# Performance work log

Measured on AMD Instinct MI355X. Metric: run time of the kernel, lower is better.

Reference implementation:

```python
import jax, jax.numpy as jnp
import numpy as np

N_QUMODES = 128
N_LAYERS = 8
BATCH = 131072
HBAR = 2.0  # PennyLane default.gaussian convention; vacuum covariance = I


def setup_inputs() -> dict:
    key = jax.random.key(0)
    k1, k2 = jax.random.split(key)
    inputs = jax.random.normal(k1, (BATCH, N_QUMODES), dtype=jnp.float32)
    params = jax.random.normal(k2, (N_LAYERS, 3 * N_QUMODES), dtype=jnp.float32)
    return {"inputs": inputs, "params": params}


def _rot(theta):
    # Rotation gate on (x, p): x -> c x - s p, p -> s x + c p. Shape [..., 2, 2].
    c, s = jnp.cos(theta), jnp.sin(theta)
    return jnp.stack([jnp.stack([c, -s], -1), jnp.stack([s, c], -1)], -2)


def _build_symplectic(params):
    """Compose the full 2N x 2N symplectic matrix for all layers.

    Per layer: local per-mode blocks R(th2) @ Sq(r) @ R(th1), then a fixed
    chain of pi/4 beamsplitters on modes (0,1),(1,2),...  Quadrature ordering
    is interleaved: (x0, p0, x1, p1, ...).
    """
    N, L = N_QUMODES, N_LAYERS
    p = params.reshape(L, N, 3)
    th1, r, th2 = p[..., 0], p[..., 1], p[..., 2]
    z = jnp.zeros_like(r)
    sq = jnp.stack([jnp.stack([jnp.exp(-r), z], -1),
                    jnp.stack([z, jnp.exp(r)], -1)], -2)  # [L, N, 2, 2]
    blk = jnp.einsum('lnab,lnbc,lncd->lnad', _rot(th2), sq, _rot(th1))

    # Fixed beamsplitter chain matrix C (theta = pi/4, phi = 0).
    t = float(np.cos(np.pi / 4))
    rr = float(np.sin(np.pi / 4))
    BS4 = jnp.array([[t, 0., -rr, 0.],
                     [0., t, 0., -rr],
                     [rr, 0., t, 0.],
                     [0., rr, 0., t]], dtype=params.dtype)
    C = jnp.eye(2 * N, dtype=params.dtype)
    for i in range(N - 1):
        C = C.at[2 * i:2 * i + 4, :].set(BS4 @ C[2 * i:2 * i + 4, :])

    idx = jnp.arange(N)
    S = jnp.eye(2 * N, dtype=params.dtype)
    for l in range(L):
        D = jnp.zeros((N, 2, N, 2), params.dtype).at[idx, :, idx, :].set(blk[l])
        S = C @ (D.reshape(2 * N, 2 * N) @ S)
    return S


def reference(inputs, params):
    """Batched Gaussian simulation of the CV QNN; returns <n_i> per sample."""
    S = _build_symplectic(params)
    B, N = inputs.shape[0], N_QUMODES
    # Displacement(a, 0): mu_x += sqrt(2*hbar) * a = 2a for hbar = 2.
    mu0 = jnp.zeros((B, 2 * N), inputs.dtype).at[:, 0::2].set(2.0 * inputs)
    mu = mu0 @ S.T                      # [B, 2N]
    V = S @ S.T                         # vacuum cov = I -> V = S S^T
    dV = jnp.diagonal(V)
    dsum = dV[0::2] + dV[1::2]          # V_xx + V_pp per mode, [N]
    n = (dsum[None, :] + mu[:, 0::2] ** 2 + mu[:, 1::2] ** 2) / (2.0 * HBAR) - 0.5
    return n
```

## Files before the change

kernel.cpp:

```cpp
#include <hip/hip_runtime.h>


#define BATCH 131072

typedef __attribute__((ext_vector_type(8))) short bf16x8;
typedef __attribute__((ext_vector_type(4))) float f32x4;

#define MFMA(a, b, c) __builtin_amdgcn_mfma_f32_16x16x32_bf16(a, b, c, 0, 0, 0)

__device__ __forceinline__ unsigned short f2bf(float f) {
  unsigned int u = __float_as_uint(f);
  u += 0x7FFFu + ((u >> 16) & 1u);
  return (unsigned short)(u >> 16);
}
__device__ __forceinline__ float bf2f(unsigned short h) {
  return __uint_as_float(((unsigned int)h) << 16);
}
__device__ __forceinline__ void pack8(const float* v, uint4& hv, uint4& lv) {
  unsigned int hw[4], lw[4];
#pragma unroll
  for (int p = 0; p < 4; ++p) {
    unsigned short h0 = f2bf(v[2 * p]), h1 = f2bf(v[2 * p + 1]);
    unsigned short l0 = f2bf(v[2 * p] - bf2f(h0)), l1 = f2bf(v[2 * p + 1] - bf2f(h1));
    hw[p] = (unsigned int)h0 | ((unsigned int)h1 << 16);
    lw[p] = (unsigned int)l0 | ((unsigned int)l1 << 16);
  }
  hv = make_uint4(hw[0], hw[1], hw[2], hw[3]);
  lv = make_uint4(lw[0], lw[1], lw[2], lw[3]);
}

__global__ __launch_bounds__(256) void build_m(const float* __restrict__ params,
                                               unsigned short* __restrict__ Mhi,
                                               unsigned short* __restrict__ Mlo) {
  int bx = blockIdx.x;
  int l = bx >> 8;
  int idx = bx & 255;
  int t = threadIdx.x;
  int i, j;
  if (l & 1) { i = idx; j = t; } else { j = idx; i = t; }
  int a = i >> 1, nn = j >> 1;
  float cx;
  if (a < 127) {
    if (nn == 0) cx = exp2f(-0.5f * (float)(a + 1));
    else if (nn <= a) cx = exp2f(-0.5f * (float)(a - nn + 2));
    else if (nn == a + 1) cx = -0.70710678118654752f;
    else cx = 0.0f;
  } else {
    cx = (nn == 0) ? exp2f(-63.5f) : exp2f(-0.5f * (float)(128 - nn));
  }
  const float* p = params + l * 384 + nn * 3;
  float th1 = p[0], r = p[1], th2 = p[2];
  float c1 = cosf(th1), s1 = sinf(th1);
  float c2 = cosf(th2), s2 = sinf(th2);
  float em = expf(-r), ep = expf(r);
  float bb;
  if (i & 1) bb = (j & 1) ? (-s2 * s1 * em + c2 * c1 * ep) : (s2 * c1 * em + c2 * s1 * ep);
  else       bb = (j & 1) ? (-c2 * s1 * em - s2 * c1 * ep) : (c2 * c1 * em - s2 * s1 * ep);
  float v = cx * bb;
  unsigned short hi = f2bf(v);
  unsigned short lo = f2bf(v - bf2f(hi));
  int off = l * 65536 + ((l & 1) ? (i * 256 + j) : (j * 256 + i));
  Mhi[off] = hi;
  Mlo[off] = lo;
}

#define PSTR 40
__global__ __launch_bounds__(256) void matprod(
    const unsigned short* __restrict__ Lhi_base, const unsigned short* __restrict__ Llo_base,
    const unsigned short* __restrict__ Rhi_base, const unsigned short* __restrict__ Rlo_base,
    unsigned short* __restrict__ Ohi, unsigned short* __restrict__ Olo,
    float* __restrict__ Sout, int final_mode) {
  __shared__ __align__(16) char lds_raw[4 * 128 * PSTR * 2];
  unsigned short* sLhi = (unsigned short*)lds_raw;
  unsigned short* sLlo = sLhi + 128 * PSTR;
  unsigned short* sRhi = sLlo + 128 * PSTR;
  unsigned short* sRlo = sRhi + 128 * PSTR;
  float* sEp = (float*)lds_raw;

  int bx = blockIdx.x;
  int pair = bx >> 2, tile = bx & 3;
  int tr = tile >> 1, tc = tile & 1;
  const unsigned short* Lhi = Lhi_base + (2 * pair + 1) * 65536;
  const unsigned short* Llo = Llo_base + (2 * pair + 1) * 65536;
  const unsigned short* Rhi = Rhi_base + (2 * pair) * 65536;
  const unsigned short* Rlo = Rlo_base + (2 * pair) * 65536;

  int t = threadIdx.x;
  int lane = t & 63, w = t >> 6;
  int wr = (w >> 1) * 64, wc = (w & 1) * 64;
  int l15 = lane & 15, q = lane >> 4;

  f32x4 acc[4][4];
#pragma unroll
  for (int a = 0; a < 4; ++a)
#pragma unroll
    for (int b = 0; b < 4; ++b) acc[a][b] = (f32x4){0.f, 0.f, 0.f, 0.f};

  for (int kc = 0; kc < 256; kc += 32) {
    __syncthreads();
#pragma unroll
    for (int it = 0; it < 2; ++it) {
      int e = it * 2048 + t * 8;
      int row = e >> 5, k = e & 31;
      *(uint4*)(sLhi + row * PSTR + k) = *(const uint4*)(Lhi + (tr * 128 + row) * 256 + kc + k);
      *(uint4*)(sLlo + row * PSTR + k) = *(const uint4*)(Llo + (tr * 128 + row) * 256 + kc + k);
      *(uint4*)(sRhi + row * PSTR + k) = *(const uint4*)(Rhi + (tc * 128 + row) * 256 + kc + k);
      *(uint4*)(sRlo + row * PSTR + k) = *(const uint4*)(Rlo + (tc * 128 + row) * 256 + kc + k);
    }
    __syncthreads();
    int kb = q * 8;
    bf16x8 afh[4], afl[4], bfh[4], bfl[4];
#pragma unroll
    for (int rt = 0; rt < 4; ++rt) {
      int r = wr + rt * 16 + l15;
      afh[rt] = *(const bf16x8*)(sLhi + r * PSTR + kb);
      afl[rt] = *(const bf16x8*)(sLlo + r * PSTR + kb);
      int n = wc + rt * 16 + l15;
      bfh[rt] = *(const bf16x8*)(sRhi + n * PSTR + kb);
      bfl[rt] = *(const bf16x8*)(sRlo + n * PSTR + kb);
    }
#pragma unroll
    for (int rt = 0; rt < 4; ++rt)
#pragma unroll
      for (int ct = 0; ct < 4; ++ct) {
        acc[rt][ct] = MFMA(afh[rt], bfh[ct], acc[rt][ct]);
        acc[rt][ct] = MFMA(afh[rt], bfl[ct], acc[rt][ct]);
        acc[rt][ct] = MFMA(afl[rt], bfh[ct], acc[rt][ct]);
      }
  }

  for (int ph = 0; ph < 2; ++ph) {
    __syncthreads();
    if (wr == ph * 64) {
#pragma unroll
      for (int rt = 0; rt < 4; ++rt)
#pragma unroll
        for (int ct = 0; ct < 4; ++ct) {
          int rl = rt * 16 + q * 4;
          int col = wc + ct * 16 + l15;
#pragma unroll
          for (int rg = 0; rg < 4; ++rg) sEp[(rl + rg) * 129 + col] = acc[rt][ct][rg];
        }
    }
    __syncthreads();
    if (final_mode) {
      int rl = t >> 2, cseg = (t & 3) * 32;
      for (int cc = 0; cc < 32; cc += 4) {
        int c = cseg + cc;
        *(float4*)(Sout + (tr * 128 + ph * 64 + rl) * 256 + tc * 128 + c) =
            make_float4(sEp[rl * 129 + c], sEp[rl * 129 + c + 1],
                        sEp[rl * 129 + c + 2], sEp[rl * 129 + c + 3]);
      }
    } else if (pair & 1) {
      int rl = t >> 2, cseg = (t & 3) * 32;
      for (int cc = 0; cc < 32; cc += 8) {
        float v[8];
#pragma unroll
        for (int jj = 0; jj < 8; ++jj) v[jj] = sEp[rl * 129 + cseg + cc + jj];
        uint4 hv, lv;
        pack8(v, hv, lv);
        int off = pair * 65536 + (tr * 128 + ph * 64 + rl) * 256 + tc * 128 + cseg + cc;
        *(uint4*)(Ohi + off) = hv;
        *(uint4*)(Olo + off) = lv;
      }
    } else {
      int col = t >> 1, rseg = (t & 1) * 32;
      for (int cc = 0; cc < 32; cc += 8) {
        float v[8];
#pragma unroll
        for (int jj = 0; jj < 8; ++jj) v[jj] = sEp[(rseg + cc + jj) * 129 + col];
        uint4 hv, lv;
        pack8(v, hv, lv);
        int off = pair * 65536 + (tc * 128 + col) * 256 + tr * 128 + ph * 64 + rseg + cc;
        *(uint4*)(Ohi + off) = hv;
        *(uint4*)(Olo + off) = lv;
      }
    }
  }
}

__global__ __launch_bounds__(64) void pack_w(const float* __restrict__ S,
                                             unsigned short* __restrict__ Whi,
                                             unsigned short* __restrict__ Wlo,
                                             float* __restrict__ dsum) {
  int b = blockIdx.x;
  int lane = threadIdx.x;
  if (b < 64) {
    int ct = b >> 2, ks = b & 3;
    int n = ct * 16 + (lane & 15);
    int k0 = ks * 32 + (lane >> 4) * 8;
    int srow = (n < 128) ? (2 * n) : (2 * (n - 128) + 1);
    float v[8];
#pragma unroll
    for (int jj = 0; jj < 8; ++jj) v[jj] = 2.0f * S[srow * 256 + 2 * (k0 + jj)];
    uint4 hv, lv;
    pack8(v, hv, lv);
    int off = ((ct * 4 + ks) * 64 + lane) * 8;
    *(uint4*)(Whi + off) = hv;
    *(uint4*)(Wlo + off) = lv;
  } else {
    int i = (b - 64) * 64 + lane;
    const float* r0 = S + (2 * i) * 256;
    const float* r1 = r0 + 256;
    float s = 0.f;
    for (int k = 0; k < 256; ++k) s += r0[k] * r0[k] + r1[k] * r1[k];
    dsum[i] = s;
  }
}

__global__ __launch_bounds__(256) void qnn_gemm(
    const float* __restrict__ A, const unsigned short* __restrict__ Whi,
    const unsigned short* __restrict__ Wlo, const float* __restrict__ dsum,
    float* __restrict__ out) {
  __shared__ unsigned short sAhi[64 * 136];
  __shared__ unsigned short sAlo[64 * 136];
  int t = threadIdx.x;
  int lane = t & 63, w = t >> 6;
  int wr = w >> 1, wc = w & 1;
  int l15 = lane & 15, q = lane >> 4;
  long brow0 = (long)blockIdx.x * 64;

#pragma unroll
  for (int it = 0; it < 8; ++it) {
    int e = it * 1024 + t * 4;
    int row = e >> 7, k = e & 127;
    float4 v = *(const float4*)(A + (brow0 + row) * 128 + k);
    unsigned short h0 = f2bf(v.x), h1 = f2bf(v.y), h2 = f2bf(v.z), h3 = f2bf(v.w);
    unsigned short l0 = f2bf(v.x - bf2f(h0)), l1 = f2bf(v.y - bf2f(h1));
    unsigned short l2 = f2bf(v.z - bf2f(h2)), l3 = f2bf(v.w - bf2f(h3));
    *(uint2*)(sAhi + row * 136 + k) =
        make_uint2((unsigned)h0 | ((unsigned)h1 << 16), (unsigned)h2 | ((unsigned)h3 << 16));
    *(uint2*)(sAlo + row * 136 + k) =
        make_uint2((unsigned)l0 | ((unsigned)l1 << 16), (unsigned)l2 | ((unsigned)l3 << 16));
  }
  __syncthreads();

  f32x4 acc[2][4][2];
#pragma unroll
  for (int rt = 0; rt < 2; ++rt)
#pragma unroll
    for (int qq = 0; qq < 4; ++qq)
#pragma unroll
      for (int xp = 0; xp < 2; ++xp) acc[rt][qq][xp] = (f32x4){0.f, 0.f, 0.f, 0.f};

#pragma unroll
  for (int ks = 0; ks < 4; ++ks) {
    int kb = ks * 32 + q * 8;
    bf16x8 ah[2], al[2];
#pragma unroll
    for (int rt = 0; rt < 2; ++rt) {
      int row = wr * 32 + rt * 16 + l15;
      ah[rt] = *(const bf16x8*)(sAhi + row * 136 + kb);
      al[rt] = *(const bf16x8*)(sAlo + row * 136 + kb);
    }
#pragma unroll
    for (int qq = 0; qq < 4; ++qq)
#pragma unroll
      for (int xp = 0; xp < 2; ++xp) {
        int ct = wc * 4 + qq + 8 * xp;
        int off = ((ct * 4 + ks) * 64 + lane) * 8;
        bf16x8 bh = *(const bf16x8*)(Whi + off);
        bf16x8 bl = *(const bf16x8*)(Wlo + off);
#pragma unroll
        for (int rt = 0; rt < 2; ++rt) {
          acc[rt][qq][xp] = MFMA(ah[rt], bh, acc[rt][qq][xp]);
          acc[rt][qq][xp] = MFMA(ah[rt], bl, acc[rt][qq][xp]);
          acc[rt][qq][xp] = MFMA(al[rt], bh, acc[rt][qq][xp]);
        }
      }
  }

#pragma unroll
  for (int qq = 0; qq < 4; ++qq) {
    int i = (wc * 4 + qq) * 16 + l15;
    float ds = dsum[i];
#pragma unroll
    for (int rt = 0; rt < 2; ++rt) {
      long row0 = brow0 + wr * 32 + rt * 16 + q * 4;
      f32x4 ax = acc[rt][qq][0];
      f32x4 ap = acc[rt][qq][1];
#pragma unroll
      for (int rg = 0; rg < 4; ++rg) {
        float val = 0.25f * (ds + ax[rg] * ax[rg] + ap[rg] * ap[rg]) - 0.5f;
        out[(row0 + rg) * 128 + i] = val;
      }
    }
  }
}

extern "C" void kernel_launch(void* const* d_in, const int* in_sizes, int n_in,
                              void* d_out, int out_size, void* d_ws, size_t ws_size,
                              hipStream_t stream) {
  const float* inputs = (const float*)d_in[0];
  const float* params = (const float*)d_in[1];
  float* out = (float*)d_out;

  unsigned short* Mhi = (unsigned short*)d_ws;
  unsigned short* Mlo = Mhi + 8 * 65536;
  unsigned short* Phi = Mlo + 8 * 65536;
  unsigned short* Plo = Phi + 4 * 65536;
  unsigned short* Qhi = Plo + 4 * 65536;
  unsigned short* Qlo = Qhi + 2 * 65536;
  float* S = (float*)(Qlo + 2 * 65536);
  unsigned short* Whi = (unsigned short*)(S + 65536);
  unsigned short* Wlo = Whi + 65536;
  float* dsum = (float*)(Wlo + 65536);

  build_m<<<2048, 256, 0, stream>>>(params, Mhi, Mlo);
  matprod<<<16, 256, 0, stream>>>(Mhi, Mlo, Mhi, Mlo, Phi, Plo, nullptr, 0);
  matprod<<<8, 256, 0, stream>>>(Phi, Plo, Phi, Plo, Qhi, Qlo, nullptr, 0);
  matprod<<<4, 256, 0, stream>>>(Qhi, Qlo, Qhi, Qlo, nullptr, nullptr, S, 1);
  pack_w<<<66, 64, 0, stream>>>(S, Whi, Wlo, dsum);
  qnn_gemm<<<2048, 256, 0, stream>>>(inputs, Whi, Wlo, dsum, out);
}
```

Baseline: 184.5 us.

## Fuse prep kernels with grid barriers and drop hi/lo split in final GEMM

Merges build_m, the three matprod stages and pack_w into one persistent 64-block kernel that uses atomic global barriers between stages. Each wave now computes a 16x64 product tile straight from global memory instead of staging tiles in LDS. The batch GEMM drops the bf16 hi/lo error-compensation split for both inputs and weights, so it issues a third of the MFMAs and half the LDS traffic. The dsum reduction is parallelised with shuffles. Accuracy drops to plain bf16 in the main GEMM, and the spin barrier relies on all 64 blocks being resident at once.

```diff
diff --git a/kernel.cpp b/kernel.cpp
--- a/kernel.cpp
+++ b/kernel.cpp
@@ -2,6 +2,7 @@
 
 
 #define BATCH 131072
+#define NB 64
 
 typedef __attribute__((ext_vector_type(8))) short bf16x8;
 typedef __attribute__((ext_vector_type(4))) float f32x4;
@@ -16,204 +17,173 @@
 __device__ __forceinline__ float bf2f(unsigned short h) {
   return __uint_as_float(((unsigned int)h) << 16);
 }
-__device__ __forceinline__ void pack8(const float* v, uint4& hv, uint4& lv) {
-  unsigned int hw[4], lw[4];
-#pragma unroll
-  for (int p = 0; p < 4; ++p) {
-    unsigned short h0 = f2bf(v[2 * p]), h1 = f2bf(v[2 * p + 1]);
-    unsigned short l0 = f2bf(v[2 * p] - bf2f(h0)), l1 = f2bf(v[2 * p + 1] - bf2f(h1));
-    hw[p] = (unsigned int)h0 | ((unsigned int)h1 << 16);
-    lw[p] = (unsigned int)l0 | ((unsigned int)l1 << 16);
-  }
-  hv = make_uint4(hw[0], hw[1], hw[2], hw[3]);
-  lv = make_uint4(lw[0], lw[1], lw[2], lw[3]);
-}
-
-__global__ __launch_bounds__(256) void build_m(const float* __restrict__ params,
-                                               unsigned short* __restrict__ Mhi,
-                                               unsigned short* __restrict__ Mlo) {
-  int bx = blockIdx.x;
-  int l = bx >> 8;
-  int idx = bx & 255;
-  int t = threadIdx.x;
-  int i, j;
-  if (l & 1) { i = idx; j = t; } else { j = idx; i = t; }
-  int a = i >> 1, nn = j >> 1;
-  float cx;
-  if (a < 127) {
-    if (nn == 0) cx = exp2f(-0.5f * (float)(a + 1));
-    else if (nn <= a) cx = exp2f(-0.5f * (float)(a - nn + 2));
-    else if (nn == a + 1) cx = -0.70710678118654752f;
-    else cx = 0.0f;
-  } else {
-    cx = (nn == 0) ? exp2f(-63.5f) : exp2f(-0.5f * (float)(128 - nn));
-  }
-  const float* p = params + l * 384 + nn * 3;
-  float th1 = p[0], r = p[1], th2 = p[2];
-  float c1 = cosf(th1), s1 = sinf(th1);
-  float c2 = cosf(th2), s2 = sinf(th2);
-  float em = expf(-r), ep = expf(r);
-  float bb;
-  if (i & 1) bb = (j & 1) ? (-s2 * s1 * em + c2 * c1 * ep) : (s2 * c1 * em + c2 * s1 * ep);
-  else       bb = (j & 1) ? (-c2 * s1 * em - s2 * c1 * ep) : (c2 * c1 * em - s2 * s1 * ep);
-  float v = cx * bb;
-  unsigned short hi = f2bf(v);
-  unsigned short lo = f2bf(v - bf2f(hi));
-  int off = l * 65536 + ((l & 1) ? (i * 256 + j) : (j * 256 + i));
-  Mhi[off] = hi;
-  Mlo[off] = lo;
-}
-
-#define PSTR 40
-__global__ __launch_bounds__(256) void matprod(
-    const unsigned short* __restrict__ Lhi_base, const unsigned short* __restrict__ Llo_base,
-    const unsigned short* __restrict__ Rhi_base, const unsigned short* __restrict__ Rlo_base,
-    unsigned short* __restrict__ Ohi, unsigned short* __restrict__ Olo,
-    float* __restrict__ Sout, int final_mode) {
-  __shared__ __align__(16) char lds_raw[4 * 128 * PSTR * 2];
-  unsigned short* sLhi = (unsigned short*)lds_raw;
-  unsigned short* sLlo = sLhi + 128 * PSTR;
-  unsigned short* sRhi = sLlo + 128 * PSTR;
-  unsigned short* sRlo = sRhi + 128 * PSTR;
-  float* sEp = (float*)lds_raw;
-
-  int bx = blockIdx.x;
-  int pair = bx >> 2, tile = bx & 3;
-  int tr = tile >> 1, tc = tile & 1;
-  const unsigned short* Lhi = Lhi_base + (2 * pair + 1) * 65536;
-  const unsigned short* Llo = Llo_base + (2 * pair + 1) * 65536;
-  const unsigned short* Rhi = Rhi_base + (2 * pair) * 65536;
-  const unsigned short* Rlo = Rlo_base + (2 * pair) * 65536;
-
+
+__device__ __forceinline__ void gbar(unsigned int* ctr) {
+  __syncthreads();
+  if (threadIdx.x == 0) {
+    __threadfence();
+    __hip_atomic_fetch_add(ctr, 1u, __ATOMIC_ACQ_REL, __HIP_MEMORY_SCOPE_AGENT);
+    while (__hip_atomic_load(ctr, __ATOMIC_ACQUIRE, __HIP_MEMORY_SCOPE_AGENT) < (unsigned)NB)
+      __builtin_amdgcn_s_sleep(1);
+  }
+  __syncthreads();
+  __threadfence();
+}
+
+__device__ void prod_subunit(const unsigned short* __restrict__ Lh,
+                             const unsigned short* __restrict__ Ll,
+                             const unsigned short* __restrict__ Rh,
+                             const unsigned short* __restrict__ Rl,
+                             int r0, int c0,
+                             unsigned short* __restrict__ Oh,
+                             unsigned short* __restrict__ Ol,
+                             int row_major, float* __restrict__ Sout) {
+  int lane = threadIdx.x & 63;
+  int l15 = lane & 15, q = lane >> 4;
+  f32x4 acc[4];
+#pragma unroll
+  for (int ct = 0; ct < 4; ++ct) acc[ct] = (f32x4){0.f, 0.f, 0.f, 0.f};
+#pragma unroll
+  for (int kc = 0; kc < 256; kc += 32) {
+    int k = kc + q * 8;
+    bf16x8 ah = *(const bf16x8*)(Lh + (r0 + l15) * 256 + k);
+    bf16x8 al = *(const bf16x8*)(Ll + (r0 + l15) * 256 + k);
+#pragma unroll
+    for (int ct = 0; ct < 4; ++ct) {
+      int n = c0 + ct * 16 + l15;
+      bf16x8 bh = *(const bf16x8*)(Rh + n * 256 + k);
+      bf16x8 bl = *(const bf16x8*)(Rl + n * 256 + k);
+      acc[ct] = MFMA(ah, bh, acc[ct]);
+      acc[ct] = MFMA(ah, bl, acc[ct]);
+      acc[ct] = MFMA(al, bh, acc[ct]);
+    }
+  }
+#pragma unroll
+  for (int ct = 0; ct < 4; ++ct) {
+    int j = c0 + ct * 16 + l15;
+#pragma unroll
+    for (int rg = 0; rg < 4; ++rg) {
+      int i = r0 + q * 4 + rg;
+      float v = acc[ct][rg];
+      if (Sout) {
+        Sout[i * 256 + j] = v;
+      } else {
+        unsigned short hi = f2bf(v);
+        unsigned short lo = f2bf(v - bf2f(hi));
+        int off = row_major ? (i * 256 + j) : (j * 256 + i);
+        Oh[off] = hi;
+        Ol[off] = lo;
+      }
+    }
+  }
+}
+
+__global__ __launch_bounds__(256) void prep(const float* __restrict__ params,
+                                            unsigned int* __restrict__ ctr,
+                                            unsigned short* __restrict__ Mhi,
+                                            unsigned short* __restrict__ Mlo,
+                                            unsigned short* __restrict__ Phi,
+                                            unsigned short* __restrict__ Plo,
+                                            unsigned short* __restrict__ Qhi,
+                                            unsigned short* __restrict__ Qlo,
+                                            float* __restrict__ S,
+                                            unsigned short* __restrict__ Wb,
+                                            float* __restrict__ dsum) {
   int t = threadIdx.x;
   int lane = t & 63, w = t >> 6;
-  int wr = (w >> 1) * 64, wc = (w & 1) * 64;
-  int l15 = lane & 15, q = lane >> 4;
-
-  f32x4 acc[4][4];
-#pragma unroll
-  for (int a = 0; a < 4; ++a)
-#pragma unroll
-    for (int b = 0; b < 4; ++b) acc[a][b] = (f32x4){0.f, 0.f, 0.f, 0.f};
-
-  for (int kc = 0; kc < 256; kc += 32) {
-    __syncthreads();
-#pragma unroll
-    for (int it = 0; it < 2; ++it) {
-      int e = it * 2048 + t * 8;
-      int row = e >> 5, k = e & 31;
-      *(uint4*)(sLhi + row * PSTR + k) = *(const uint4*)(Lhi + (tr * 128 + row) * 256 + kc + k);
-      *(uint4*)(sLlo + row * PSTR + k) = *(const uint4*)(Llo + (tr * 128 + row) * 256 + kc + k);
-      *(uint4*)(sRhi + row * PSTR + k) = *(const uint4*)(Rhi + (tc * 128 + row) * 256 + kc + k);
-      *(uint4*)(sRlo + row * PSTR + k) = *(const uint4*)(Rlo + (tc * 128 + row) * 256 + kc + k);
-    }
-    __syncthreads();
-    int kb = q * 8;
-    bf16x8 afh[4], afl[4], bfh[4], bfl[4];
-#pragma unroll
-    for (int rt = 0; rt < 4; ++rt) {
-      int r = wr + rt * 16 + l15;
-      afh[rt] = *(const bf16x8*)(sLhi + r * PSTR + kb);
-      afl[rt] = *(const bf16x8*)(sLlo + r * PSTR + kb);
-      int n = wc + rt * 16 + l15;
-      bfh[rt] = *(const bf16x8*)(sRhi + n * PSTR + kb);
-      bfl[rt] = *(const bf16x8*)(sRlo + n * PSTR + kb);
-    }
-#pragma unroll
-    for (int rt = 0; rt < 4; ++rt)
-#pragma unroll
-      for (int ct = 0; ct < 4; ++ct) {
-        acc[rt][ct] = MFMA(afh[rt], bfh[ct], acc[rt][ct]);
-        acc[rt][ct] = MFMA(afh[rt], bfl[ct], acc[rt][ct]);
-        acc[rt][ct] = MFMA(afl[rt], bfh[ct], acc[rt][ct]);
-      }
-  }
-
-  for (int ph = 0; ph < 2; ++ph) {
-    __syncthreads();
-    if (wr == ph * 64) {
-#pragma unroll
-      for (int rt = 0; rt < 4; ++rt)
-#pragma unroll
-        for (int ct = 0; ct < 4; ++ct) {
-          int rl = rt * 16 + q * 4;
-          int col = wc + ct * 16 + l15;
-#pragma unroll
-          for (int rg = 0; rg < 4; ++rg) sEp[(rl + rg) * 129 + col] = acc[rt][ct][rg];
-        }
-    }
-    __syncthreads();
-    if (final_mode) {
-      int rl = t >> 2, cseg = (t & 3) * 32;
-      for (int cc = 0; cc < 32; cc += 4) {
-        int c = cseg + cc;
-        *(float4*)(Sout + (tr * 128 + ph * 64 + rl) * 256 + tc * 128 + c) =
-            make_float4(sEp[rl * 129 + c], sEp[rl * 129 + c + 1],
-                        sEp[rl * 129 + c + 2], sEp[rl * 129 + c + 3]);
-      }
-    } else if (pair & 1) {
-      int rl = t >> 2, cseg = (t & 3) * 32;
-      for (int cc = 0; cc < 32; cc += 8) {
-        float v[8];
-#pragma unroll
-        for (int jj = 0; jj < 8; ++jj) v[jj] = sEp[rl * 129 + cseg + cc + jj];
-        uint4 hv, lv;
-        pack8(v, hv, lv);
-        int off = pair * 65536 + (tr * 128 + ph * 64 + rl) * 256 + tc * 128 + cseg + cc;
-        *(uint4*)(Ohi + off) = hv;
-        *(uint4*)(Olo + off) = lv;
-      }
+  int gw = blockIdx.x * 4 + w;
+
+#pragma unroll 1
+  for (int it = 0; it < 32; ++it) {
+    int task = blockIdx.x * 32 + it;
+    int l = task >> 8, idx = task & 255;
+    int i, j;
+    if (l & 1) { i = idx; j = t; } else { j = idx; i = t; }
+    int a = i >> 1, nn = j >> 1;
+    float cx;
+    if (a < 127) {
+      if (nn == 0) cx = exp2f(-0.5f * (float)(a + 1));
+      else if (nn <= a) cx = exp2f(-0.5f * (float)(a - nn + 2));
+      else if (nn == a + 1) cx = -0.70710678118654752f;
+      else cx = 0.0f;
     } else {
-      int col = t >> 1, rseg = (t & 1) * 32;
-      for (int cc = 0; cc < 32; cc += 8) {
-        float v[8];
-#pragma unroll
-        for (int jj = 0; jj < 8; ++jj) v[jj] = sEp[(rseg + cc + jj) * 129 + col];
-        uint4 hv, lv;
-        pack8(v, hv, lv);
-        int off = pair * 65536 + (tc * 128 + col) * 256 + tr * 128 + ph * 64 + rseg + cc;
-        *(uint4*)(Ohi + off) = hv;
-        *(uint4*)(Olo + off) = lv;
-      }
-    }
-  }
-}
-
-__global__ __launch_bounds__(64) void pack_w(const float* __restrict__ S,
-                                             unsigned short* __restrict__ Whi,
-                                             unsigned short* __restrict__ Wlo,
-                                             float* __restrict__ dsum) {
-  int b = blockIdx.x;
-  int lane = threadIdx.x;
-  if (b < 64) {
-    int ct = b >> 2, ks = b & 3;
+      cx = (nn == 0) ? exp2f(-63.5f) : exp2f(-0.5f * (float)(128 - nn));
+    }
+    const float* p = params + l * 384 + nn * 3;
+    float th1 = p[0], r = p[1], th2 = p[2];
+    float c1 = cosf(th1), s1 = sinf(th1);
+    float c2 = cosf(th2), s2 = sinf(th2);
+    float em = expf(-r), ep = expf(r);
+    float bb;
+    if (i & 1) bb = (j & 1) ? (-s2 * s1 * em + c2 * c1 * ep) : (s2 * c1 * em + c2 * s1 * ep);
+    else       bb = (j & 1) ? (-c2 * s1 * em - s2 * c1 * ep) : (c2 * c1 * em - s2 * s1 * ep);
+    float v = cx * bb;
+    unsigned short hi = f2bf(v);
+    unsigned short lo = f2bf(v - bf2f(hi));
+    int off = l * 65536 + ((l & 1) ? (i * 256 + j) : (j * 256 + i));
+    Mhi[off] = hi;
+    Mlo[off] = lo;
+  }
+  gbar(ctr + 0);
+
+  {
+    int p = gw >> 6, ul = gw & 63;
+    prod_subunit(Mhi + (2 * p + 1) * 65536, Mlo + (2 * p + 1) * 65536,
+                 Mhi + (2 * p) * 65536, Mlo + (2 * p) * 65536,
+                 (ul >> 2) * 16, (ul & 3) * 64,
+                 Phi + p * 65536, Plo + p * 65536, p & 1, nullptr);
+  }
+  gbar(ctr + 1);
+
+  if (gw < 128) {
+    int p = gw >> 6, ul = gw & 63;
+    prod_subunit(Phi + (2 * p + 1) * 65536, Plo + (2 * p + 1) * 65536,
+                 Phi + (2 * p) * 65536, Plo + (2 * p) * 65536,
+                 (ul >> 2) * 16, (ul & 3) * 64,
+                 Qhi + p * 65536, Qlo + p * 65536, p & 1, nullptr);
+  }
+  gbar(ctr + 2);
+
+  if (gw < 64) {
+    int ul = gw & 63;
+    prod_subunit(Qhi + 65536, Qlo + 65536, Qhi, Qlo,
+                 (ul >> 2) * 16, (ul & 3) * 64, nullptr, nullptr, 0, S);
+  }
+  gbar(ctr + 3);
+
+  if (gw < 64) {
+    int ct = gw >> 2, ks = gw & 3;
     int n = ct * 16 + (lane & 15);
     int k0 = ks * 32 + (lane >> 4) * 8;
     int srow = (n < 128) ? (2 * n) : (2 * (n - 128) + 1);
-    float v[8];
-#pragma unroll
-    for (int jj = 0; jj < 8; ++jj) v[jj] = 2.0f * S[srow * 256 + 2 * (k0 + jj)];
-    uint4 hv, lv;
-    pack8(v, hv, lv);
-    int off = ((ct * 4 + ks) * 64 + lane) * 8;
-    *(uint4*)(Whi + off) = hv;
-    *(uint4*)(Wlo + off) = lv;
-  } else {
-    int i = (b - 64) * 64 + lane;
+    unsigned int wd[4];
+#pragma unroll
+    for (int p2 = 0; p2 < 4; ++p2) {
+      unsigned short h0 = f2bf(2.0f * S[srow * 256 + 2 * (k0 + 2 * p2)]);
+      unsigned short h1 = f2bf(2.0f * S[srow * 256 + 2 * (k0 + 2 * p2 + 1)]);
+      wd[p2] = (unsigned int)h0 | ((unsigned int)h1 << 16);
+    }
+    *(uint4*)(Wb + ((ct * 4 + ks) * 64 + lane) * 8) = make_uint4(wd[0], wd[1], wd[2], wd[3]);
+  }
+  __shared__ float sred[4];
+  for (int h = 0; h < 2; ++h) {
+    int i = blockIdx.x * 2 + h;
     const float* r0 = S + (2 * i) * 256;
     const float* r1 = r0 + 256;
-    float s = 0.f;
-    for (int k = 0; k < 256; ++k) s += r0[k] * r0[k] + r1[k] * r1[k];
-    dsum[i] = s;
+    float s = r0[t] * r0[t] + r1[t] * r1[t];
+#pragma unroll
+    for (int off = 32; off; off >>= 1) s += __shfl_down(s, off);
+    __syncthreads();
+    if (lane == 0) sred[w] = s;
+    __syncthreads();
+    if (t == 0) dsum[i] = sred[0] + sred[1] + sred[2] + sred[3];
   }
 }
 
 __global__ __launch_bounds__(256) void qnn_gemm(
-    const float* __restrict__ A, const unsigned short* __restrict__ Whi,
-    const unsigned short* __restrict__ Wlo, const float* __restrict__ dsum,
-    float* __restrict__ out) {
-  __shared__ unsigned short sAhi[64 * 136];
-  __shared__ unsigned short sAlo[64 * 136];
+    const float* __restrict__ A, const unsigned short* __restrict__ Wb,
+    const float* __restrict__ dsum, float* __restrict__ out) {
+  __shared__ unsigned short sA[64 * 136];
   int t = threadIdx.x;
   int lane = t & 63, w = t >> 6;
   int wr = w >> 1, wc = w & 1;
@@ -224,14 +194,10 @@
   for (int it = 0; it < 8; ++it) {
     int e = it * 1024 + t * 4;
     int row = e >> 7, k = e & 127;
-    float4 v = *(const float4*)(A + (brow0 + row) * 128 + k);
-    unsigned short h0 = f2bf(v.x), h1 = f2bf(v.y), h2 = f2bf(v.z), h3 = f2bf(v.w);
-    unsigned short l0 = f2bf(v.x - bf2f(h0)), l1 = f2bf(v.y - bf2f(h1));
-    unsigned short l2 = f2bf(v.z - bf2f(h2)), l3 = f2bf(v.w - bf2f(h3));
-    *(uint2*)(sAhi + row * 136 + k) =
-        make_uint2((unsigned)h0 | ((unsigned)h1 << 16), (unsigned)h2 | ((unsigned)h3 << 16));
-    *(uint2*)(sAlo + row * 136 + k) =
-        make_uint2((unsigned)l0 | ((unsigned)l1 << 16), (unsigned)l2 | ((unsigned)l3 << 16));
+    float4 v = *(const float4*)(A + brow0 * 128 + e);
+    *(uint2*)(sA + row * 136 + k) = make_uint2(
+        (unsigned int)f2bf(v.x) | ((unsigned int)f2bf(v.y) << 16),
+        (unsigned int)f2bf(v.z) | ((unsigned int)f2bf(v.w) << 16));
   }
   __syncthreads();
 
@@ -246,27 +212,16 @@
 #pragma unroll
   for (int ks = 0; ks < 4; ++ks) {
     int kb = ks * 32 + q * 8;
-    bf16x8 ah[2], al[2];
-#pragma unroll
-    for (int rt = 0; rt < 2; ++rt) {
-      int row = wr * 32 + rt * 16 + l15;
-      ah[rt] = *(const bf16x8*)(sAhi + row * 136 + kb);
-      al[rt] = *(const bf16x8*)(sAlo + row * 136 + kb);
-    }
+    bf16x8 a0 = *(const bf16x8*)(sA + (wr * 32 + l15) * 136 + kb);
+    bf16x8 a1 = *(const bf16x8*)(sA + (wr * 32 + 16 + l15) * 136 + kb);
 #pragma unroll
     for (int qq = 0; qq < 4; ++qq)
 #pragma unroll
       for (int xp = 0; xp < 2; ++xp) {
         int ct = wc * 4 + qq + 8 * xp;
-        int off = ((ct * 4 + ks) * 64 + lane) * 8;
-        bf16x8 bh = *(const bf16x8*)(Whi + off);
-        bf16x8 bl = *(const bf16x8*)(Wlo + off);
-#pragma unroll
-        for (int rt = 0; rt < 2; ++rt) {
-          acc[rt][qq][xp] = MFMA(ah[rt], bh, acc[rt][qq][xp]);
-          acc[rt][qq][xp] = MFMA(ah[rt], bl, acc[rt][qq][xp]);
-          acc[rt][qq][xp] = MFMA(al[rt], bh, acc[rt][qq][xp]);
-        }
+        bf16x8 b = *(const bf16x8*)(Wb + ((ct * 4 + ks) * 64 + lane) * 8);
+        acc[0][qq][xp] = MFMA(a0, b, acc[0][qq][xp]);
+        acc[1][qq][xp] = MFMA(a1, b, acc[1][qq][xp]);
       }
   }
 
@@ -295,21 +250,19 @@
   const float* params = (const float*)d_in[1];
   float* out = (float*)d_out;
 
-  unsigned short* Mhi = (unsigned short*)d_ws;
+  unsigned int* ctr = (unsigned int*)d_ws;
+  unsigned short* base = (unsigned short*)((char*)d_ws + 256);
+  unsigned short* Mhi = base;
   unsigned short* Mlo = Mhi + 8 * 65536;
   unsigned short* Phi = Mlo + 8 * 65536;
   unsigned short* Plo = Phi + 4 * 65536;
   unsigned short* Qhi = Plo + 4 * 65536;
   unsigned short* Qlo = Qhi + 2 * 65536;
   float* S = (float*)(Qlo + 2 * 65536);
-  unsigned short* Whi = (unsigned short*)(S + 65536);
-  unsigned short* Wlo = Whi + 65536;
-  float* dsum = (float*)(Wlo + 65536);
-
-  build_m<<<2048, 256, 0, stream>>>(params, Mhi, Mlo);
-  matprod<<<16, 256, 0, stream>>>(Mhi, Mlo, Mhi, Mlo, Phi, Plo, nullptr, 0);
-  matprod<<<8, 256, 0, stream>>>(Phi, Plo, Phi, Plo, Qhi, Qlo, nullptr, 0);
-  matprod<<<4, 256, 0, stream>>>(Qhi, Qlo, Qhi, Qlo, nullptr, nullptr, S, 1);
-  pack_w<<<66, 64, 0, stream>>>(S, Whi, Wlo, dsum);
-  qnn_gemm<<<2048, 256, 0, stream>>>(inputs, Whi, Wlo, dsum, out);
-}
+  unsigned short* Wb = (unsigned short*)(S + 65536);
+  float* dsum = (float*)(Wb + 65536);
+
+  hipMemsetAsync(d_ws, 0, 256, stream);
+  prep<<<NB, 256, 0, stream>>>(params, ctr, Mhi, Mlo, Phi, Plo, Qhi, Qlo, S, Wb, dsum);
+  qnn_gemm<<<2048, 256, 0, stream>>>(inputs, Wb, dsum, out);
+}
```

Measured after the change: 220.9 us. 19.7% more time.

## Fuse matrix build into first product, fuse W packing, drop split-bf16 in batch GEMM

Applied to the files above, without the earlier changes.

Per-layer matrix construction now happens inside the first pairwise product kernel, and W packing plus the dsum reduction move into the final product kernel's epilogue. This removes two launches and the intermediate M/S buffers. The big batch GEMM now uses a single bf16 term instead of the hi/lo three-MFMA split, and uses nontemporal loads and stores. That cuts MFMA work and LDS traffic by about 3x, at the cost of accuracy on the inputs and on W.

```diff
diff --git a/kernel.cpp b/kernel.cpp
--- a/kernel.cpp
+++ b/kernel.cpp
@@ -2,6 +2,7 @@
 
 
 #define BATCH 131072
+#define PSTR 40
 
 typedef __attribute__((ext_vector_type(8))) short bf16x8;
 typedef __attribute__((ext_vector_type(4))) float f32x4;
@@ -29,47 +30,164 @@
   lv = make_uint4(lw[0], lw[1], lw[2], lw[3]);
 }
 
-__global__ __launch_bounds__(256) void build_m(const float* __restrict__ params,
-                                               unsigned short* __restrict__ Mhi,
-                                               unsigned short* __restrict__ Mlo) {
+__device__ __forceinline__ float cxf(const float* powc, int a, int nn) {
+  if (a < 127) {
+    if (nn == 0) return powc[a + 1];
+    if (nn <= a) return powc[a - nn + 2];
+    if (nn == a + 1) return -0.70710678118654752f;
+    return 0.0f;
+  }
+  return (nn == 0) ? powc[127] : powc[128 - nn];
+}
+
+__global__ __launch_bounds__(256) void l1_prod(const float* __restrict__ params,
+                                               unsigned short* __restrict__ Phi,
+                                               unsigned short* __restrict__ Plo) {
+  __shared__ __align__(16) char lds_raw[4 * 128 * PSTR * 2];
+  __shared__ float blkA[128][4];
+  __shared__ float blkB[128][4];
+  __shared__ float powc[132];
+  unsigned short* sLhi = (unsigned short*)lds_raw;
+  unsigned short* sLlo = sLhi + 128 * PSTR;
+  unsigned short* sRhi = sLlo + 128 * PSTR;
+  unsigned short* sRlo = sRhi + 128 * PSTR;
+  float* sEp = (float*)lds_raw;
+
   int bx = blockIdx.x;
-  int l = bx >> 8;
-  int idx = bx & 255;
+  int pair = bx >> 2, tile = bx & 3;
+  int tr = tile >> 1, tc = tile & 1;
   int t = threadIdx.x;
-  int i, j;
-  if (l & 1) { i = idx; j = t; } else { j = idx; i = t; }
-  int a = i >> 1, nn = j >> 1;
-  float cx;
-  if (a < 127) {
-    if (nn == 0) cx = exp2f(-0.5f * (float)(a + 1));
-    else if (nn <= a) cx = exp2f(-0.5f * (float)(a - nn + 2));
-    else if (nn == a + 1) cx = -0.70710678118654752f;
-    else cx = 0.0f;
-  } else {
-    cx = (nn == 0) ? exp2f(-63.5f) : exp2f(-0.5f * (float)(128 - nn));
-  }
-  const float* p = params + l * 384 + nn * 3;
-  float th1 = p[0], r = p[1], th2 = p[2];
-  float c1 = cosf(th1), s1 = sinf(th1);
-  float c2 = cosf(th2), s2 = sinf(th2);
-  float em = expf(-r), ep = expf(r);
-  float bb;
-  if (i & 1) bb = (j & 1) ? (-s2 * s1 * em + c2 * c1 * ep) : (s2 * c1 * em + c2 * s1 * ep);
-  else       bb = (j & 1) ? (-c2 * s1 * em - s2 * c1 * ep) : (c2 * c1 * em - s2 * s1 * ep);
-  float v = cx * bb;
-  unsigned short hi = f2bf(v);
-  unsigned short lo = f2bf(v - bf2f(hi));
-  int off = l * 65536 + ((l & 1) ? (i * 256 + j) : (j * 256 + i));
-  Mhi[off] = hi;
-  Mlo[off] = lo;
-}
-
-#define PSTR 40
+  int lane = t & 63, w = t >> 6;
+  int wr = (w >> 1) * 64, wc = (w & 1) * 64;
+  int l15 = lane & 15, q = lane >> 4;
+
+  {
+    int l = (t < 128) ? (2 * pair + 1) : (2 * pair);
+    int nn = t & 127;
+    const float* p = params + l * 384 + nn * 3;
+    float th1 = p[0], r = p[1], th2 = p[2];
+    float c1 = cosf(th1), s1 = sinf(th1);
+    float c2 = cosf(th2), s2 = sinf(th2);
+    float em = expf(-r), ep = expf(r);
+    float* dst = (t < 128) ? blkA[nn] : blkB[nn];
+    dst[0] = c2 * c1 * em - s2 * s1 * ep;
+    dst[1] = -c2 * s1 * em - s2 * c1 * ep;
+    dst[2] = s2 * c1 * em + c2 * s1 * ep;
+    dst[3] = -s2 * s1 * em + c2 * c1 * ep;
+    if (t < 132) powc[t] = exp2f(-0.5f * (float)t);
+  }
+
+  f32x4 acc[4][4];
+#pragma unroll
+  for (int a = 0; a < 4; ++a)
+#pragma unroll
+    for (int b = 0; b < 4; ++b) acc[a][b] = (f32x4){0.f, 0.f, 0.f, 0.f};
+
+  for (int kc = 0; kc < 256; kc += 32) {
+    __syncthreads();
+#pragma unroll
+    for (int it = 0; it < 2; ++it) {
+      int e = it * 2048 + t * 8;
+      int row = e >> 5, k0 = e & 31;
+      {
+        int i = tr * 128 + row;
+        int a = i >> 1;
+        float vv[8];
+#pragma unroll
+        for (int jj = 0; jj < 8; ++jj) {
+          int j = kc + k0 + jj;
+          int nn = j >> 1;
+          vv[jj] = cxf(powc, a, nn) * blkA[nn][(i & 1) * 2 + (j & 1)];
+        }
+        uint4 hv, lv;
+        pack8(vv, hv, lv);
+        *(uint4*)(sLhi + row * PSTR + k0) = hv;
+        *(uint4*)(sLlo + row * PSTR + k0) = lv;
+      }
+      {
+        int j = tc * 128 + row;
+        int nn = j >> 1;
+        float b0 = blkB[nn][0 + (j & 1)];
+        float b1 = blkB[nn][2 + (j & 1)];
+        float vv[8];
+#pragma unroll
+        for (int jj = 0; jj < 8; ++jj) {
+          int i = kc + k0 + jj;
+          vv[jj] = cxf(powc, i >> 1, nn) * ((i & 1) ? b1 : b0);
+        }
+        uint4 hv, lv;
+        pack8(vv, hv, lv);
+        *(uint4*)(sRhi + row * PSTR + k0) = hv;
+        *(uint4*)(sRlo + row * PSTR + k0) = lv;
+      }
+    }
+    __syncthreads();
+    int kb = q * 8;
+    bf16x8 afh[4], afl[4], bfh[4], bfl[4];
+#pragma unroll
+    for (int rt = 0; rt < 4; ++rt) {
+      int r = wr + rt * 16 + l15;
+      afh[rt] = *(const bf16x8*)(sLhi + r * PSTR + kb);
+      afl[rt] = *(const bf16x8*)(sLlo + r * PSTR + kb);
+      int n = wc + rt * 16 + l15;
+      bfh[rt] = *(const bf16x8*)(sRhi + n * PSTR + kb);
+      bfl[rt] = *(const bf16x8*)(sRlo + n * PSTR + kb);
+    }
+#pragma unroll
+    for (int rt = 0; rt < 4; ++rt)
+#pragma unroll
+      for (int ct = 0; ct < 4; ++ct) {
+        acc[rt][ct] = MFMA(afh[rt], bfh[ct], acc[rt][ct]);
+        acc[rt][ct] = MFMA(afh[rt], bfl[ct], acc[rt][ct]);
+        acc[rt][ct] = MFMA(afl[rt], bfh[ct], acc[rt][ct]);
+      }
+  }
+
+  for (int ph = 0; ph < 2; ++ph) {
+    __syncthreads();
+    if (wr == ph * 64) {
+#pragma unroll
+      for (int rt = 0; rt < 4; ++rt)
+#pragma unroll
+        for (int ct = 0; ct < 4; ++ct) {
+          int rl = rt * 16 + q * 4;
+          int col = wc + ct * 16 + l15;
+#pragma unroll
+          for (int rg = 0; rg < 4; ++rg) sEp[(rl + rg) * 129 + col] = acc[rt][ct][rg];
+        }
+    }
+    __syncthreads();
+    if (pair & 1) {
+      int rl = t >> 2, cseg = (t & 3) * 32;
+      for (int cc = 0; cc < 32; cc += 8) {
+        float v[8];
+#pragma unroll
+        for (int jj = 0; jj < 8; ++jj) v[jj] = sEp[rl * 129 + cseg + cc + jj];
+        uint4 hv, lv;
+        pack8(v, hv, lv);
+        int off = pair * 65536 + (tr * 128 + ph * 64 + rl) * 256 + tc * 128 + cseg + cc;
+        *(uint4*)(Phi + off) = hv;
+        *(uint4*)(Plo + off) = lv;
+      }
+    } else {
+      int col = t >> 1, rseg = (t & 1) * 32;
+      for (int cc = 0; cc < 32; cc += 8) {
+        float v[8];
+#pragma unroll
+        for (int jj = 0; jj < 8; ++jj) v[jj] = sEp[(rseg + cc + jj) * 129 + col];
+        uint4 hv, lv;
+        pack8(v, hv, lv);
+        int off = pair * 65536 + (tc * 128 + col) * 256 + tr * 128 + ph * 64 + rseg + cc;
+        *(uint4*)(Phi + off) = hv;
+        *(uint4*)(Plo + off) = lv;
+      }
+    }
+  }
+}
+
 __global__ __launch_bounds__(256) void matprod(
     const unsigned short* __restrict__ Lhi_base, const unsigned short* __restrict__ Llo_base,
-    const unsigned short* __restrict__ Rhi_base, const unsigned short* __restrict__ Rlo_base,
-    unsigned short* __restrict__ Ohi, unsigned short* __restrict__ Olo,
-    float* __restrict__ Sout, int final_mode) {
+    unsigned short* __restrict__ Ohi, unsigned short* __restrict__ Olo) {
   __shared__ __align__(16) char lds_raw[4 * 128 * PSTR * 2];
   unsigned short* sLhi = (unsigned short*)lds_raw;
   unsigned short* sLlo = sLhi + 128 * PSTR;
@@ -82,8 +200,8 @@
   int tr = tile >> 1, tc = tile & 1;
   const unsigned short* Lhi = Lhi_base + (2 * pair + 1) * 65536;
   const unsigned short* Llo = Llo_base + (2 * pair + 1) * 65536;
-  const unsigned short* Rhi = Rhi_base + (2 * pair) * 65536;
-  const unsigned short* Rlo = Rlo_base + (2 * pair) * 65536;
+  const unsigned short* Rhi = Lhi_base + (2 * pair) * 65536;
+  const unsigned short* Rlo = Llo_base + (2 * pair) * 65536;
 
   int t = threadIdx.x;
   int lane = t & 63, w = t >> 6;
@@ -143,15 +261,7 @@
         }
     }
     __syncthreads();
-    if (final_mode) {
-      int rl = t >> 2, cseg = (t & 3) * 32;
-      for (int cc = 0; cc < 32; cc += 4) {
-        int c = cseg + cc;
-        *(float4*)(Sout + (tr * 128 + ph * 64 + rl) * 256 + tc * 128 + c) =
-            make_float4(sEp[rl * 129 + c], sEp[rl * 129 + c + 1],
-                        sEp[rl * 129 + c + 2], sEp[rl * 129 + c + 3]);
-      }
-    } else if (pair & 1) {
+    if (pair & 1) {
       int rl = t >> 2, cseg = (t & 3) * 32;
       for (int cc = 0; cc < 32; cc += 8) {
         float v[8];
@@ -179,41 +289,124 @@
   }
 }
 
-__global__ __launch_bounds__(64) void pack_w(const float* __restrict__ S,
-                                             unsigned short* __restrict__ Whi,
-                                             unsigned short* __restrict__ Wlo,
-                                             float* __restrict__ dsum) {
-  int b = blockIdx.x;
-  int lane = threadIdx.x;
-  if (b < 64) {
-    int ct = b >> 2, ks = b & 3;
-    int n = ct * 16 + (lane & 15);
-    int k0 = ks * 32 + (lane >> 4) * 8;
-    int srow = (n < 128) ? (2 * n) : (2 * (n - 128) + 1);
-    float v[8];
-#pragma unroll
-    for (int jj = 0; jj < 8; ++jj) v[jj] = 2.0f * S[srow * 256 + 2 * (k0 + jj)];
-    uint4 hv, lv;
-    pack8(v, hv, lv);
-    int off = ((ct * 4 + ks) * 64 + lane) * 8;
-    *(uint4*)(Whi + off) = hv;
-    *(uint4*)(Wlo + off) = lv;
-  } else {
-    int i = (b - 64) * 64 + lane;
-    const float* r0 = S + (2 * i) * 256;
-    const float* r1 = r0 + 256;
-    float s = 0.f;
-    for (int k = 0; k < 256; ++k) s += r0[k] * r0[k] + r1[k] * r1[k];
-    dsum[i] = s;
+__global__ __launch_bounds__(256) void l3_fused(
+    const unsigned short* __restrict__ Qhi, const unsigned short* __restrict__ Qlo,
+    unsigned short* __restrict__ Wb, float* __restrict__ dsum_part) {
+  __shared__ __align__(16) char lds_raw[4 * 128 * PSTR * 2];
+  unsigned short* sLhi = (unsigned short*)lds_raw;
+  unsigned short* sLlo = sLhi + 128 * PSTR;
+  unsigned short* sRhi = sLlo + 128 * PSTR;
+  unsigned short* sRlo = sRhi + 128 * PSTR;
+  float* sEp = (float*)lds_raw;
+
+  int tile = blockIdx.x & 3;
+  int tr = tile >> 1, tc = tile & 1;
+  const unsigned short* Lhi = Qhi + 65536;
+  const unsigned short* Llo = Qlo + 65536;
+  const unsigned short* Rhi = Qhi;
+  const unsigned short* Rlo = Qlo;
+
+  int t = threadIdx.x;
+  int lane = t & 63, w = t >> 6;
+  int wr = (w >> 1) * 64, wc = (w & 1) * 64;
+  int l15 = lane & 15, q = lane >> 4;
+
+  f32x4 acc[4][4];
+#pragma unroll
+  for (int a = 0; a < 4; ++a)
+#pragma unroll
+    for (int b = 0; b < 4; ++b) acc[a][b] = (f32x4){0.f, 0.f, 0.f, 0.f};
+
+  for (int kc = 0; kc < 256; kc += 32) {
+    __syncthreads();
+#pragma unroll
+    for (int it = 0; it < 2; ++it) {
+      int e = it * 2048 + t * 8;
+      int row = e >> 5, k = e & 31;
+      *(uint4*)(sLhi + row * PSTR + k) = *(const uint4*)(Lhi + (tr * 128 + row) * 256 + kc + k);
+      *(uint4*)(sLlo + row * PSTR + k) = *(const uint4*)(Llo + (tr * 128 + row) * 256 + kc + k);
+      *(uint4*)(sRhi + row * PSTR + k) = *(const uint4*)(Rhi + (tc * 128 + row) * 256 + kc + k);
+      *(uint4*)(sRlo + row * PSTR + k) = *(const uint4*)(Rlo + (tc * 128 + row) * 256 + kc + k);
+    }
+    __syncthreads();
+    int kb = q * 8;
+    bf16x8 afh[4], afl[4], bfh[4], bfl[4];
+#pragma unroll
+    for (int rt = 0; rt < 4; ++rt) {
+      int r = wr + rt * 16 + l15;
+      afh[rt] = *(const bf16x8*)(sLhi + r * PSTR + kb);
+      afl[rt] = *(const bf16x8*)(sLlo + r * PSTR + kb);
+      int n = wc + rt * 16 + l15;
+      bfh[rt] = *(const bf16x8*)(sRhi + n * PSTR + kb);
+      bfl[rt] = *(const bf16x8*)(sRlo + n * PSTR + kb);
+    }
+#pragma unroll
+    for (int rt = 0; rt < 4; ++rt)
+#pragma unroll
+      for (int ct = 0; ct < 4; ++ct) {
+        acc[rt][ct] = MFMA(afh[rt], bfh[ct], acc[rt][ct]);
+        acc[rt][ct] = MFMA(afh[rt], bfl[ct], acc[rt][ct]);
+        acc[rt][ct] = MFMA(afl[rt], bfh[ct], acc[rt][ct]);
+      }
+  }
+
+  for (int ph = 0; ph < 2; ++ph) {
+    __syncthreads();
+    if (wr == ph * 64) {
+#pragma unroll
+      for (int rt = 0; rt < 4; ++rt)
+#pragma unroll
+        for (int ct = 0; ct < 4; ++ct) {
+          int rl = rt * 16 + q * 4;
+          int col = wc + ct * 16 + l15;
+#pragma unroll
+          for (int rg = 0; rg < 4; ++rg) sEp[(rl + rg) * 129 + col] = acc[rt][ct][rg];
+        }
+    }
+    __syncthreads();
+    int rbase = tr * 128 + ph * 64;
+    int ctbase = tr * 4 + ph * 2;
+#pragma unroll
+    for (int ci = 0; ci < 2; ++ci) {
+      int cell = w * 2 + ci;
+      int c2 = cell >> 1;
+      int ct = ctbase + (c2 & 1) + ((c2 & 2) ? 8 : 0);
+      int ks = 2 * tc + (cell & 1);
+      int n = ct * 16 + l15;
+      int srow = (n < 128) ? (2 * n) : (2 * (n - 128) + 1);
+      int lr = srow - rbase;
+      int lc0 = (cell & 1) * 64 + q * 16;
+      float v[8];
+#pragma unroll
+      for (int jj = 0; jj < 8; ++jj) v[jj] = 2.0f * sEp[lr * 129 + lc0 + 2 * jj];
+      unsigned int wd[4];
+#pragma unroll
+      for (int p2 = 0; p2 < 4; ++p2)
+        wd[p2] = (unsigned int)f2bf(v[2 * p2]) | ((unsigned int)f2bf(v[2 * p2 + 1]) << 16);
+      *(uint4*)(Wb + ((ct * 4 + ks) * 64 + lane) * 8) = make_uint4(wd[0], wd[1], wd[2], wd[3]);
+    }
+    {
+      int ii = t >> 3, s = t & 7;
+      int c0 = s * 16;
+      float sum = 0.f;
+#pragma unroll
+      for (int c = 0; c < 16; ++c) {
+        float x = sEp[(2 * ii) * 129 + c0 + c];
+        float y = sEp[(2 * ii + 1) * 129 + c0 + c];
+        sum += x * x + y * y;
+      }
+      sum += __shfl_down(sum, 4, 8);
+      sum += __shfl_down(sum, 2, 8);
+      sum += __shfl_down(sum, 1, 8);
+      if (s == 0) dsum_part[tc * 128 + (rbase >> 1) + ii] = sum;
+    }
   }
 }
 
 __global__ __launch_bounds__(256) void qnn_gemm(
-    const float* __restrict__ A, const unsigned short* __restrict__ Whi,
-    const unsigned short* __restrict__ Wlo, const float* __restrict__ dsum,
-    float* __restrict__ out) {
-  __shared__ unsigned short sAhi[64 * 136];
-  __shared__ unsigned short sAlo[64 * 136];
+    const float* __restrict__ A, const unsigned short* __restrict__ Wb,
+    const float* __restrict__ dsum_part, float* __restrict__ out) {
+  __shared__ unsigned short sA[64 * 136];
   int t = threadIdx.x;
   int lane = t & 63, w = t >> 6;
   int wr = w >> 1, wc = w & 1;
@@ -224,14 +417,10 @@
   for (int it = 0; it < 8; ++it) {
     int e = it * 1024 + t * 4;
     int row = e >> 7, k = e & 127;
-    float4 v = *(const float4*)(A + (brow0 + row) * 128 + k);
-    unsigned short h0 = f2bf(v.x), h1 = f2bf(v.y), h2 = f2bf(v.z), h3 = f2bf(v.w);
-    unsigned short l0 = f2bf(v.x - bf2f(h0)), l1 = f2bf(v.y - bf2f(h1));
-    unsigned short l2 = f2bf(v.z - bf2f(h2)), l3 = f2bf(v.w - bf2f(h3));
-    *(uint2*)(sAhi + row * 136 + k) =
-        make_uint2((unsigned)h0 | ((unsigned)h1 << 16), (unsigned)h2 | ((unsigned)h3 << 16));
-    *(uint2*)(sAlo + row * 136 + k) =
-        make_uint2((unsigned)l0 | ((unsigned)l1 << 16), (unsigned)l2 | ((unsigned)l3 << 16));
+    f32x4 v = __builtin_nontemporal_load((const f32x4*)(A + brow0 * 128 + e));
+    *(uint2*)(sA + row * 136 + k) = make_uint2(
+        (unsigned int)f2bf(v.x) | ((unsigned int)f2bf(v.y) << 16),
+        (unsigned int)f2bf(v.z) | ((unsigned int)f2bf(v.w) << 16));
   }
   __syncthreads();
 
@@ -246,34 +435,23 @@
 #pragma unroll
   for (int ks = 0; ks < 4; ++ks) {
     int kb = ks * 32 + q * 8;
-    bf16x8 ah[2], al[2];
-#pragma unroll
-    for (int rt = 0; rt < 2; ++rt) {
-      int row = wr * 32 + rt * 16 + l15;
-      ah[rt] = *(const bf16x8*)(sAhi + row * 136 + kb);
-      al[rt] = *(const bf16x8*)(sAlo + row * 136 + kb);
-    }
+    bf16x8 a0 = *(const bf16x8*)(sA + (wr * 32 + l15) * 136 + kb);
+    bf16x8 a1 = *(const bf16x8*)(sA + (wr * 32 + 16 + l15) * 136 + kb);
 #pragma unroll
     for (int qq = 0; qq < 4; ++qq)
 #pragma unroll
       for (int xp = 0; xp < 2; ++xp) {
         int ct = wc * 4 + qq + 8 * xp;
-        int off = ((ct * 4 + ks) * 64 + lane) * 8;
-        bf16x8 bh = *(const bf16x8*)(Whi + off);
-        bf16x8 bl = *(const bf16x8*)(Wlo + off);
-#pragma unroll
-        for (int rt = 0; rt < 2; ++rt) {
-          acc[rt][qq][xp] = MFMA(ah[rt], bh, acc[rt][qq][xp]);
-          acc[rt][qq][xp] = MFMA(ah[rt], bl, acc[rt][qq][xp]);
-          acc[rt][qq][xp] = MFMA(al[rt], bh, acc[rt][qq][xp]);
-        }
+        bf16x8 b = *(const bf16x8*)(Wb + ((ct * 4 + ks) * 64 + lane) * 8);
+        acc[0][qq][xp] = MFMA(a0, b, acc[0][qq][xp]);
+        acc[1][qq][xp] = MFMA(a1, b, acc[1][qq][xp]);
       }
   }
 
 #pragma unroll
   for (int qq = 0; qq < 4; ++qq) {
     int i = (wc * 4 + qq) * 16 + l15;
-    float ds = dsum[i];
+    float ds = dsum_part[i] + dsum_part[128 + i];
 #pragma unroll
     for (int rt = 0; rt < 2; ++rt) {
       long row0 = brow0 + wr * 32 + rt * 16 + q * 4;
@@ -282,7 +460,7 @@
 #pragma unroll
       for (int rg = 0; rg < 4; ++rg) {
         float val = 0.25f * (ds + ax[rg] * ax[rg] + ap[rg] * ap[rg]) - 0.5f;
-        out[(row0 + rg) * 128 + i] = val;
+        __builtin_nontemporal_store(val, &out[(row0 + rg) * 128 + i]);
       }
     }
   }
@@ -295,21 +473,15 @@
   const float* params = (const float*)d_in[1];
   float* out = (float*)d_out;
 
-  unsigned short* Mhi = (unsigned short*)d_ws;
-  unsigned short* Mlo = Mhi + 8 * 65536;
-  unsigned short* Phi = Mlo + 8 * 65536;
+  unsigned short* Phi = (unsigned short*)d_ws;
   unsigned short* Plo = Phi + 4 * 65536;
   unsigned short* Qhi = Plo + 4 * 65536;
   unsigned short* Qlo = Qhi + 2 * 65536;
-  float* S = (float*)(Qlo + 2 * 65536);
-  unsigned short* Whi = (unsigned short*)(S + 65536);
-  unsigned short* Wlo = Whi + 65536;
-  float* dsum = (float*)(Wlo + 65536);
-
-  build_m<<<2048, 256, 0, stream>>>(params, Mhi, Mlo);
-  matprod<<<16, 256, 0, stream>>>(Mhi, Mlo, Mhi, Mlo, Phi, Plo, nullptr, 0);
-  matprod<<<8, 256, 0, stream>>>(Phi, Plo, Phi, Plo, Qhi, Qlo, nullptr, 0);
-  matprod<<<4, 256, 0, stream>>>(Qhi, Qlo, Qhi, Qlo, nullptr, nullptr, S, 1);
-  pack_w<<<66, 64, 0, stream>>>(S, Whi, Wlo, dsum);
-  qnn_gemm<<<2048, 256, 0, stream>>>(inputs, Whi, Wlo, dsum, out);
-}
+  unsigned short* Wb = Qlo + 2 * 65536;
+  float* dsum_part = (float*)(Wb + 65536);
+
+  l1_prod<<<16, 256, 0, stream>>>(params, Phi, Plo);
+  matprod<<<8, 256, 0, stream>>>(Phi, Plo, Qhi, Qlo);
+  l3_fused<<<4, 256, 0, stream>>>(Qhi, Qlo, Wb, dsum_part);
+  qnn_gemm<<<2048, 256, 0, stream>>>(inputs, Wb, dsum_part, out);
+}
```

After: 184.2 us. Within noise of the previous version (-0.2%).
